# Kernel optimization log

Hardware: AMD Instinct MI355X
Metric: run time of the kernel (lower is better)

The kernel has to match this reference:

```python
import jax, jax.numpy as jnp
import numpy as np
import math

N_TOK = 8192; IN_DIM = 1024; D = 512; HEADS = 8; DH = D // HEADS
M = D // 2; ITERS = 6; SCALE = DH ** -0.5; KRES = 33; NCLS = 2
EPS = 1e-5


def ln(x, g, b):
    mu = jnp.mean(x, -1, keepdims=True)
    var = jnp.var(x, -1, keepdims=True)
    return (x - mu) * jax.lax.rsqrt(var + EPS) * g + b


def moore_penrose_pinv(x):
    # Newton-Schulz iterative pseudo-inverse (lucidrains nystrom-attention)
    col = jnp.abs(x).sum(-1).max()
    row = jnp.abs(x).sum(-2).max()
    z = jnp.swapaxes(x, -1, -2) / (col * row)
    I = jnp.eye(x.shape[-1], dtype=x.dtype)
    for _ in range(ITERS):
        xz = x @ z
        z = 0.25 * z @ (13 * I - xz @ (15 * I - xz @ (7 * I - xz)))
    return z


def nystrom_attn(x, qkv_w, out_w, out_b, conv_w):
    b, n, _ = x.shape
    pad = (-n) % M  # pad at FRONT so seq len divisible by num_landmarks
    xp = jnp.pad(x, ((0, 0), (pad, 0), (0, 0)))
    Np = n + pad
    q, k, v = jnp.split(xp @ qkv_w, 3, axis=-1)
    tohead = lambda t: t.reshape(b, Np, HEADS, DH).transpose(0, 2, 1, 3)  # bhnd
    q = tohead(q) * SCALE; k = tohead(k); v = tohead(v)
    l = Np // M
    q_l = q.reshape(b, HEADS, M, l, DH).mean(3)  # landmark means, bhmd
    k_l = k.reshape(b, HEADS, M, l, DH).mean(3)
    a1 = jax.nn.softmax(jnp.einsum('bhnd,bhmd->bhnm', q, k_l), -1)
    a2 = jax.nn.softmax(jnp.einsum('bhnd,bhmd->bhnm', q_l, k_l), -1)
    a3 = jax.nn.softmax(jnp.einsum('bhmd,bhnd->bhmn', q_l, k), -1)
    out = (a1 @ moore_penrose_pinv(a2)) @ (a3 @ v)
    pc = KRES // 2  # depthwise residual conv over sequence dim (groups=heads)
    out = out + jax.lax.conv_general_dilated(
        v, conv_w, (1, 1), [(pc, pc), (0, 0)],
        dimension_numbers=('NCHW', 'OIHW', 'NCHW'), feature_group_count=HEADS)
    out = out.transpose(0, 2, 1, 3).reshape(b, Np, D)
    return (out @ out_w + out_b)[:, -n:]


def ppeg(x, Hs, Ws, w7, b7, w5, b5, w3, b3):
    b, _, C = x.shape
    cls_tok, feat = x[:, :1], x[:, 1:]
    f = feat.transpose(0, 2, 1).reshape(b, C, Hs, Ws)
    def dw(w, bb, p):
        return jax.lax.conv_general_dilated(
            f, w, (1, 1), [(p, p), (p, p)],
            dimension_numbers=('NCHW', 'OIHW', 'NCHW'),
            feature_group_count=C) + bb[None, :, None, None]
    y = f + dw(w7, b7, 3) + dw(w5, b5, 2) + dw(w3, b3, 1)
    y = y.reshape(b, C, Hs * Ws).transpose(0, 2, 1)
    return jnp.concatenate([cls_tok, y], axis=1)


def setup_inputs() -> dict:
    key = jax.random.key(0)
    ks = jax.random.split(key, 16)
    s = 0.02
    return {
        'x': jax.random.normal(ks[0], (N_TOK, IN_DIM), jnp.float32),
        'fc1_w': jax.random.normal(ks[1], (IN_DIM, D), jnp.float32) * s,
        'fc1_b': jnp.zeros((D,), jnp.float32),
        'cls_token': jax.random.normal(ks[2], (1, 1, D), jnp.float32),
        'ln1_g': jnp.ones((D,), jnp.float32), 'ln1_b': jnp.zeros((D,), jnp.float32),
        'qkv1_w': jax.random.normal(ks[3], (D, 3 * D), jnp.float32) * s,
        'out1_w': jax.random.normal(ks[4], (D, D), jnp.float32) * s,
        'out1_b': jnp.zeros((D,), jnp.float32),
        'conv1_w': jax.random.normal(ks[5], (HEADS, 1, KRES, 1), jnp.float32) * s,
        'ln2_g': jnp.ones((D,), jnp.float32), 'ln2_b': jnp.zeros((D,), jnp.float32),
        'qkv2_w': jax.random.normal(ks[6], (D, 3 * D), jnp.float32) * s,
        'out2_w': jax.random.normal(ks[7], (D, D), jnp.float32) * s,
        'out2_b': jnp.zeros((D,), jnp.float32),
        'conv2_w': jax.random.normal(ks[8], (HEADS, 1, KRES, 1), jnp.float32) * s,
        'pg7_w': jax.random.normal(ks[9], (D, 1, 7, 7), jnp.float32) * s,
        'pg7_b': jnp.zeros((D,), jnp.float32),
        'pg5_w': jax.random.normal(ks[10], (D, 1, 5, 5), jnp.float32) * s,
        'pg5_b': jnp.zeros((D,), jnp.float32),
        'pg3_w': jax.random.normal(ks[11], (D, 1, 3, 3), jnp.float32) * s,
        'pg3_b': jnp.zeros((D,), jnp.float32),
        'norm_g': jnp.ones((D,), jnp.float32), 'norm_b': jnp.zeros((D,), jnp.float32),
        'fc2_w': jax.random.normal(ks[12], (D, NCLS), jnp.float32) * s,
        'fc2_b': jnp.zeros((NCLS,), jnp.float32),
    }


def reference(x, fc1_w, fc1_b, cls_token, ln1_g, ln1_b, qkv1_w, out1_w, out1_b,
              conv1_w, ln2_g, ln2_b, qkv2_w, out2_w, out2_b, conv2_w,
              pg7_w, pg7_b, pg5_w, pg5_b, pg3_w, pg3_b, norm_g, norm_b,
              fc2_w, fc2_b):
    h = jax.nn.relu(x[None].astype(jnp.float32) @ fc1_w + fc1_b)  # [1,N,D]
    n = h.shape[1]
    Hs = Ws = int(math.ceil(math.sqrt(n)))
    add = Hs * Ws - n
    h = jnp.concatenate([h, h[:, :add]], axis=1)  # pad to square by duplication
    h = jnp.concatenate([jnp.broadcast_to(cls_token, (1, 1, D)), h], axis=1)
    h = h + nystrom_attn(ln(h, ln1_g, ln1_b), qkv1_w, out1_w, out1_b, conv1_w)
    h = ppeg(h, Hs, Ws, pg7_w, pg7_b, pg5_w, pg5_b, pg3_w, pg3_b)
    h = h + nystrom_attn(ln(h, ln2_g, ln2_b), qkv2_w, out2_w, out2_b, conv2_w)
    emb = ln(h, norm_g, norm_b)[:, 0]  # cls embedding [1,D]
    logits = emb @ fc2_w + fc2_b
    Y_prob = jax.nn.softmax(logits, -1)
    Y_hat = jnp.argmax(logits, -1)
    return (logits, Y_prob, Y_hat, emb)
```

## Files before the change

kernel.cpp:

```cpp
#include <hip/hip_runtime.h>
#include <math.h>

#define NTOK   8192
#define INDIM  1024
#define NHEAD  8
#define N1     8282
#define NP     8448
#define PAD    166
#define LCH    33
#define SCALE  0.125f
#define HS     91
#define KSPLIT 24
#define KCH    (NP / KSPLIT)

typedef __attribute__((ext_vector_type(8))) _Float16 half8;
typedef __attribute__((ext_vector_type(8))) short short8;
typedef __attribute__((ext_vector_type(4))) float f32x4;
typedef unsigned short ushort_t;

#define GPTR(p) ((const __attribute__((address_space(1))) void*)(p))
#define LPTR(p) ((__attribute__((address_space(3))) void*)(p))

__device__ __forceinline__ ushort_t f2h(float f) {
    union { _Float16 h; ushort_t u; } v; v.h = (_Float16)f;
    return v.u;
}
__device__ __forceinline__ float h2f(ushort_t u) {
    union { ushort_t u; _Float16 h; } v; v.u = u;
    return (float)v.h;
}


__device__ __forceinline__ float blockReduceSumF(float v, float* red, int tid) {
    red[tid] = v; __syncthreads();
    for (int s = 128; s > 0; s >>= 1) {
        if (tid < s) red[tid] += red[tid + s];
        __syncthreads();
    }
    float r = red[0]; __syncthreads();
    return r;
}
__device__ __forceinline__ float blockReduceMaxF(float v, float* red, int tid) {
    red[tid] = v; __syncthreads();
    for (int s = 128; s > 0; s >>= 1) {
        if (tid < s) red[tid] = fmaxf(red[tid], red[tid + s]);
        __syncthreads();
    }
    float r = red[0]; __syncthreads();
    return r;
}

__global__ void zero_k(float* __restrict__ p)
{
    int i = blockIdx.x * 256 + threadIdx.x;
    reinterpret_cast<float4*>(p)[i] = make_float4(0.f, 0.f, 0.f, 0.f);
}

__global__ __launch_bounds__(256) void tcast_k(const float* __restrict__ w, ushort_t* __restrict__ wT,
                                               int K, int N)
{
    __shared__ float tb[32][33];
    int tx = threadIdx.x & 31, ty = threadIdx.x >> 5;
    int n0 = blockIdx.x * 32, k0 = blockIdx.y * 32;
#pragma unroll
    for (int i = 0; i < 4; ++i)
        tb[ty + i * 8][tx] = w[(size_t)(k0 + ty + i * 8) * N + n0 + tx];
    __syncthreads();
#pragma unroll
    for (int i = 0; i < 4; ++i)
        wT[(size_t)(n0 + ty + i * 8) * K + k0 + tx] = f2h(tb[tx][ty + i * 8]);
}

__global__ void bcast_k(const float* __restrict__ x, ushort_t* __restrict__ o)
{
    int i = blockIdx.x * 256 + threadIdx.x;
    float4 v = reinterpret_cast<const float4*>(x)[i];
    ushort4 u;
    u.x = f2h(v.x); u.y = f2h(v.y); u.z = f2h(v.z); u.w = f2h(v.w);
    reinterpret_cast<ushort4*>(o)[i] = u;
}

__global__ __launch_bounds__(256) void gemm_mn_f16(
    const ushort_t* __restrict__ A, const ushort_t* __restrict__ BT,
    const float* __restrict__ bias, const float* __restrict__ res,
    float* __restrict__ C, ushort_t* __restrict__ Ch,
    int Mvalid, int K, int lda, int ldb, int ldc, int relu, int qscale)
{
    __shared__ ushort_t As[128 * 32];
    __shared__ ushort_t Bs[64 * 32];
    const int tid = threadIdx.x;
    const int wave = tid >> 6, lane = tid & 63;
    const int row0 = blockIdx.y * 128, col0 = blockIdx.x * 64;
    const int wr = wave * 32;
    const int aRow = wave * 16 + (lane >> 2);
    const int aChS = (((lane & 3) ^ ((lane >> 3) & 3)) * 8);
    const int bRow = tid >> 2;
    const int bChS = (((tid & 3) ^ ((tid >> 3) & 3)) * 8);
    const int lr = lane & 15, lq = (lane >> 4) * 4;
    const int lks = (((lane >> 4) ^ ((lr >> 1) & 3)) * 8);
    f32x4 acc[2][4] = {};
    for (int k0 = 0; k0 < K; k0 += 32) {
        __syncthreads();
#pragma unroll
        for (int i = 0; i < 2; ++i) {
            const ushort_t* gp = A + (size_t)(row0 + i * 64 + aRow) * lda + k0 + aChS;
            __builtin_amdgcn_global_load_lds(GPTR(gp), LPTR(As + (i * 64 + wave * 16) * 32), 16, 0, 0);
        }
        const ushort_t* gq = BT + (size_t)(col0 + bRow) * ldb + k0 + bChS;
        __builtin_amdgcn_global_load_lds(GPTR(gq), LPTR(Bs + tid * 8), 16, 0, 0);
        __syncthreads();
        half8 af[2], bfr[4];
#pragma unroll
        for (int mi = 0; mi < 2; ++mi)
            af[mi] = *reinterpret_cast<const half8*>(&As[(wr + mi * 16 + lr) * 32 + lks]);
#pragma unroll
        for (int ni = 0; ni < 4; ++ni)
            bfr[ni] = *reinterpret_cast<const half8*>(&Bs[(ni * 16 + lr) * 32 + lks]);
#pragma unroll
        for (int mi = 0; mi < 2; ++mi)
#pragma unroll
            for (int ni = 0; ni < 4; ++ni)
                acc[mi][ni] = __builtin_amdgcn_mfma_f32_16x16x32_f16(af[mi], bfr[ni], acc[mi][ni], 0, 0, 0);
    }
#pragma unroll
    for (int mi = 0; mi < 2; ++mi) {
#pragma unroll
        for (int q = 0; q < 4; ++q) {
            int r = row0 + wr + mi * 16 + lq + q;
            if (r >= Mvalid) continue;
#pragma unroll
            for (int ni = 0; ni < 4; ++ni) {
                int c = col0 + ni * 16 + lr;
                float v = acc[mi][ni][q];
                if (bias) v += bias[c];
                if (res)  v += res[(size_t)r * ldc + c];
                if (relu) v = fmaxf(v, 0.f);
                if (Ch) {
                    if (qscale && c < 512) v *= SCALE;
                    Ch[(size_t)r * ldc + c] = f2h(v);
                } else {
                    C[(size_t)r * ldc + c] = v;
                }
            }
        }
    }
}

__global__ __launch_bounds__(256) void bgemm64_f16(
    const ushort_t* __restrict__ A, const ushort_t* __restrict__ B,
    ushort_t* __restrict__ C, float diag, float ss,
    ushort_t* __restrict__ C2, float diag2, float ss2)
{
    __shared__ ushort_t As[64 * 32];
    __shared__ ushort_t Bs[64 * 32];
    const int h = blockIdx.z;
    const ushort_t* Ah = A + (size_t)h * 65536;
    const ushort_t* Bh = B + (size_t)h * 65536;
    const int tid = threadIdx.x;
    const int wave = tid >> 6, lane = tid & 63;
    const int row0 = blockIdx.y * 64, col0 = blockIdx.x * 64;
    const int wr = (wave >> 1) * 32, wc = (wave & 1) * 32;
    const int aRow = tid >> 2;
    const int aChS = (((tid & 3) ^ ((tid >> 3) & 3)) * 8);
    const int kp = (tid >> 3) & 15, nc = tid & 7;
    const int kk = (kp * 2) ^ ((nc & 3) << 3);
    const int lr = lane & 15, lk = (lane >> 4) * 8, lq = (lane >> 4) * 4;
    const int lks = (((lane >> 4) ^ ((lr >> 1) & 3)) * 8);
    f32x4 acc[2][2] = {};
    for (int k0 = 0; k0 < 256; k0 += 32) {
        __syncthreads();
        const ushort_t* gp = Ah + (size_t)(row0 + aRow) * 256 + k0 + aChS;
        __builtin_amdgcn_global_load_lds(GPTR(gp), LPTR(As + tid * 8), 16, 0, 0);
        if (tid < 128) {
            const ushort_t* bp = Bh + (size_t)(k0 + kp * 2) * 256 + col0 + nc * 8;
            short8 v0 = *reinterpret_cast<const short8*>(bp);
            short8 v1 = *reinterpret_cast<const short8*>(bp + 256);
#pragma unroll
            for (int j = 0; j < 8; ++j) {
                unsigned int pk = ((unsigned int)(ushort_t)v1[j] << 16) | (unsigned int)(ushort_t)v0[j];
                *reinterpret_cast<unsigned int*>(&Bs[(nc * 8 + j) * 32 + kk]) = pk;
            }
        }
        __syncthreads();
        half8 af[2], bfr[2];
#pragma unroll
        for (int mi = 0; mi < 2; ++mi)
            af[mi] = *reinterpret_cast<const half8*>(&As[(wr + mi * 16 + lr) * 32 + lks]);
#pragma unroll
        for (int ni = 0; ni < 2; ++ni) {
            int nn = wc + ni * 16 + lr;
            bfr[ni] = *reinterpret_cast<const half8*>(&Bs[nn * 32 + (lk ^ (((nn >> 3) & 3) << 3))]);
        }
#pragma unroll
        for (int mi = 0; mi < 2; ++mi)
#pragma unroll
            for (int ni = 0; ni < 2; ++ni)
                acc[mi][ni] = __builtin_amdgcn_mfma_f32_16x16x32_f16(af[mi], bfr[ni], acc[mi][ni], 0, 0, 0);
    }
    ushort_t* Chp = C + (size_t)h * 65536;
#pragma unroll
    for (int mi = 0; mi < 2; ++mi)
#pragma unroll
        for (int ni = 0; ni < 2; ++ni)
#pragma unroll
            for (int q = 0; q < 4; ++q) {
                int r = row0 + wr + mi * 16 + lq + q;
                int c = col0 + wc + ni * 16 + lr;
                float v = ss * acc[mi][ni][q];
                if (r == c) v += diag;
                Chp[(size_t)r * 256 + c] = f2h(v);
                if (C2) {
                    float v2 = ss2 * acc[mi][ni][q];
                    if (r == c) v2 += diag2;
                    C2[(size_t)h * 65536 + (size_t)r * 256 + c] = f2h(v2);
                }
            }
}

__global__ __launch_bounds__(256) void hgemm_abT_k(
    const ushort_t* __restrict__ A, long sAh, int lda,
    const ushort_t* __restrict__ BT, long sBh, int ldb,
    ushort_t* __restrict__ C, long sCh, int ldc, int K,
    float* __restrict__ rsum, int sRsum)
{
    __shared__ ushort_t As[128 * 32];
    __shared__ ushort_t Bs[128 * 32];
    const int h = blockIdx.z;
    const ushort_t* Ah = A + (size_t)h * sAh;
    const ushort_t* Bh = BT + (size_t)h * sBh;
    ushort_t* Chp = C + (size_t)h * sCh;
    const int tid = threadIdx.x;
    const int wave = tid >> 6, lane = tid & 63;
    const int row0 = blockIdx.y * 128, col0 = blockIdx.x * 128;
    const int wr = (wave >> 1) * 64, wc = (wave & 1) * 64;
    const int sRow = wave * 16 + (lane >> 2);
    const int sChS = (((lane & 3) ^ ((lane >> 3) & 3)) * 8);
    const int lr = lane & 15, lq = (lane >> 4) * 4;
    const int lks = (((lane >> 4) ^ ((lr >> 1) & 3)) * 8);
    f32x4 acc[4][4] = {};
    for (int k0 = 0; k0 < K; k0 += 32) {
        __syncthreads();
#pragma unroll
        for (int i = 0; i < 2; ++i) {
            const ushort_t* gp = Ah + (size_t)(row0 + i * 64 + sRow) * lda + k0 + sChS;
            __builtin_amdgcn_global_load_lds(GPTR(gp), LPTR(As + (i * 64 + wave * 16) * 32), 16, 0, 0);
            const ushort_t* gq = Bh + (size_t)(col0 + i * 64 + sRow) * ldb + k0 + sChS;
            __builtin_amdgcn_global_load_lds(GPTR(gq), LPTR(Bs + (i * 64 + wave * 16) * 32), 16, 0, 0);
        }
        __syncthreads();
        half8 af[4], bfr[4];
#pragma unroll
        for (int mi = 0; mi < 4; ++mi)
            af[mi] = *reinterpret_cast<const half8*>(&As[(wr + mi * 16 + lr) * 32 + lks]);
#pragma unroll
        for (int ni = 0; ni < 4; ++ni)
            bfr[ni] = *reinterpret_cast<const half8*>(&Bs[(wc + ni * 16 + lr) * 32 + lks]);
#pragma unroll
        for (int mi = 0; mi < 4; ++mi)
#pragma unroll
            for (int ni = 0; ni < 4; ++ni)
                acc[mi][ni] = __builtin_amdgcn_mfma_f32_16x16x32_f16(af[mi], bfr[ni], acc[mi][ni], 0, 0, 0);
    }
#pragma unroll
    for (int mi = 0; mi < 4; ++mi)
#pragma unroll
        for (int q = 0; q < 4; ++q) {
            int r = row0 + wr + mi * 16 + lq + q;
            float s = 0.f;
#pragma unroll
            for (int ni = 0; ni < 4; ++ni) {
                float e = __expf(acc[mi][ni][q]);
                Chp[(size_t)r * ldc + col0 + wc + ni * 16 + lr] = f2h(e);
                s += e;
            }
            for (int off = 8; off; off >>= 1) s += __shfl_xor(s, off, 64);
            if (lr == 0) atomicAdd(&rsum[(size_t)h * sRsum + r], s);
        }
}

__global__ __launch_bounds__(256) void hgemm_pv_k(
    const ushort_t* __restrict__ P, const ushort_t* __restrict__ qkv16,
    float* __restrict__ part)
{
    __shared__ ushort_t As[128 * 32];
    __shared__ ushort_t Bs[64 * 32];
    const int ks = blockIdx.x, row0 = blockIdx.y * 128, h = blockIdx.z;
    const ushort_t* Ph = P + (size_t)h * 256 * NP;
    const ushort_t* V = qkv16 + 1024 + h * 64;
    const int tid = threadIdx.x;
    const int wave = tid >> 6, lane = tid & 63;
    const int wr = wave * 32;
    const int sRow = wave * 16 + (lane >> 2);
    const int sChS = (((lane & 3) ^ ((lane >> 3) & 3)) * 8);
    const int lr = lane & 15, lk = (lane >> 4) * 8, lq = (lane >> 4) * 4;
    const int lks = (((lane >> 4) ^ ((lr >> 1) & 3)) * 8);
    const int kp = (tid >> 3) & 15, nc = tid & 7;
    const int kk = (kp * 2) ^ ((nc & 3) << 3);
    f32x4 acc[2][4] = {};
    for (int k0 = ks * KCH; k0 < (ks + 1) * KCH; k0 += 32) {
        __syncthreads();
#pragma unroll
        for (int i = 0; i < 2; ++i) {
            const ushort_t* gp = Ph + (size_t)(row0 + i * 64 + sRow) * NP + k0 + sChS;
            __builtin_amdgcn_global_load_lds(GPTR(gp), LPTR(As + (i * 64 + wave * 16) * 32), 16, 0, 0);
        }
        if (tid < 128) {
            const ushort_t* bp = V + (size_t)(k0 + kp * 2) * 1536 + nc * 8;
            short8 v0 = *reinterpret_cast<const short8*>(bp);
            short8 v1 = *reinterpret_cast<const short8*>(bp + 1536);
#pragma unroll
            for (int j = 0; j < 8; ++j) {
                unsigned int pk = ((unsigned int)(ushort_t)v1[j] << 16) | (unsigned int)(ushort_t)v0[j];
                *reinterpret_cast<unsigned int*>(&Bs[(nc * 8 + j) * 32 + kk]) = pk;
            }
        }
        __syncthreads();
        half8 af[2], bfr[4];
#pragma unroll
        for (int mi = 0; mi < 2; ++mi)
            af[mi] = *reinterpret_cast<const half8*>(&As[(wr + mi * 16 + lr) * 32 + lks]);
#pragma unroll
        for (int ni = 0; ni < 4; ++ni) {
            int nn = ni * 16 + lr;
            bfr[ni] = *reinterpret_cast<const half8*>(&Bs[nn * 32 + (lk ^ (((nn >> 3) & 3) << 3))]);
        }
#pragma unroll
        for (int mi = 0; mi < 2; ++mi)
#pragma unroll
            for (int ni = 0; ni < 4; ++ni)
                acc[mi][ni] = __builtin_amdgcn_mfma_f32_16x16x32_f16(af[mi], bfr[ni], acc[mi][ni], 0, 0, 0);
    }
    float* pp = part + ((size_t)(ks * 8 + h) * 256) * 64;
#pragma unroll
    for (int mi = 0; mi < 2; ++mi)
#pragma unroll
        for (int q = 0; q < 4; ++q) {
            int r = row0 + wr + mi * 16 + lq + q;
#pragma unroll
            for (int ni = 0; ni < 4; ++ni)
                pp[(size_t)r * 64 + ni * 16 + lr] = acc[mi][ni][q];
        }
}

__global__ __launch_bounds__(256) void pv_reduce_k(const float* __restrict__ part,
                                                   const float* __restrict__ rsum,
                                                   ushort_t* __restrict__ av)
{
    int idx = blockIdx.x * 256 + threadIdx.x;
    int rc = idx >> 6;
    float s = 0.f;
#pragma unroll
    for (int ks = 0; ks < KSPLIT; ++ks)
        s += part[(size_t)ks * 131072 + idx];
    av[idx] = f2h(s / rsum[rc]);
}

__global__ __launch_bounds__(256) void wmat_k(const ushort_t* __restrict__ z,
                                              const ushort_t* __restrict__ av,
                                              ushort_t* __restrict__ W)
{
    int idx = blockIdx.x * 4 + (threadIdx.x >> 6);
    int h = idx >> 8, m = idx & 255, d = threadIdx.x & 63;
    const ushort_t* zp = z + (size_t)h * 65536 + (size_t)m * 256;
    const ushort_t* ap = av + (size_t)h * 16384 + d;
    float acc = 0.f;
    for (int j = 0; j < 256; ++j) acc += h2f(zp[j]) * h2f(ap[(size_t)j * 64]);
    W[((size_t)h * 256 + m) * 64 + d] = f2h(acc);
}

__global__ __launch_bounds__(256) void hgemm_pw_k(
    const ushort_t* __restrict__ P1, const ushort_t* __restrict__ W,
    const float* __restrict__ rsum, ushort_t* __restrict__ attn)
{
    __shared__ ushort_t As[128 * 32];
    __shared__ ushort_t Bs[64 * 32];
    const int row0 = blockIdx.y * 128, h = blockIdx.z;
    const ushort_t* Ph = P1 + (size_t)h * NP * 256;
    const ushort_t* Wh = W + (size_t)h * 16384;
    const int tid = threadIdx.x;
    const int wave = tid >> 6, lane = tid & 63;
    const int wr = wave * 32;
    const int sRow = wave * 16 + (lane >> 2);
    const int sChS = (((lane & 3) ^ ((lane >> 3) & 3)) * 8);
    const int lr = lane & 15, lk = (lane >> 4) * 8, lq = (lane >> 4) * 4;
    const int lks = (((lane >> 4) ^ ((lr >> 1) & 3)) * 8);
    const int kp = (tid >> 3) & 15, nc = tid & 7;
    const int kk = (kp * 2) ^ ((nc & 3) << 3);
    f32x4 acc[2][4] = {};
    for (int k0 = 0; k0 < 256; k0 += 32) {
        __syncthreads();
#pragma unroll
        for (int i = 0; i < 2; ++i) {
            const ushort_t* gp = Ph + (size_t)(row0 + i * 64 + sRow) * 256 + k0 + sChS;
            __builtin_amdgcn_global_load_lds(GPTR(gp), LPTR(As + (i * 64 + wave * 16) * 32), 16, 0, 0);
        }
        if (tid < 128) {
            const ushort_t* bp = Wh + (size_t)(k0 + kp * 2) * 64 + nc * 8;
            short8 v0 = *reinterpret_cast<const short8*>(bp);
            short8 v1 = *reinterpret_cast<const short8*>(bp + 64);
#pragma unroll
            for (int j = 0; j < 8; ++j) {
                unsigned int pk = ((unsigned int)(ushort_t)v1[j] << 16) | (unsigned int)(ushort_t)v0[j];
                *reinterpret_cast<unsigned int*>(&Bs[(nc * 8 + j) * 32 + kk]) = pk;
            }
        }
        __syncthreads();
        half8 af[2], bfr[4];
#pragma unroll
        for (int mi = 0; mi < 2; ++mi)
            af[mi] = *reinterpret_cast<const half8*>(&As[(wr + mi * 16 + lr) * 32 + lks]);
#pragma unroll
        for (int ni = 0; ni < 4; ++ni) {
            int nn = ni * 16 + lr;
            bfr[ni] = *reinterpret_cast<const half8*>(&Bs[nn * 32 + (lk ^ (((nn >> 3) & 3) << 3))]);
        }
#pragma unroll
        for (int mi = 0; mi < 2; ++mi)
#pragma unroll
            for (int ni = 0; ni < 4; ++ni)
                acc[mi][ni] = __builtin_amdgcn_mfma_f32_16x16x32_f16(af[mi], bfr[ni], acc[mi][ni], 0, 0, 0);
    }
#pragma unroll
    for (int mi = 0; mi < 2; ++mi)
#pragma unroll
        for (int q = 0; q < 4; ++q) {
            int t = row0 + wr + mi * 16 + lq + q;
            float inv = 1.f / rsum[(size_t)h * NP + t];
#pragma unroll
            for (int ni = 0; ni < 4; ++ni)
                attn[(size_t)t * 512 + h * 64 + ni * 16 + lr] = f2h(acc[mi][ni][q] * inv);
        }
}

__global__ void fixup_k(const float* __restrict__ cls, float* __restrict__ h)
{
    int i = blockIdx.x * 256 + threadIdx.x;
    if (i < 512) {
        h[i] = cls[i];
    } else {
        int j = i - 512;
        h[(size_t)8193 * 512 + j] = h[512 + j];
    }
}

__global__ __launch_bounds__(256) void ln_pad_k(
    const float* __restrict__ h, const float* __restrict__ g, const float* __restrict__ b,
    ushort_t* __restrict__ out)
{
    int row = blockIdx.x, tid = threadIdx.x;
    __shared__ float red[256];
    ushort_t* o = out + (size_t)row * 512;
    if (row < PAD) { o[tid] = 0; o[tid + 256] = 0; return; }
    const float* x = h + (size_t)(row - PAD) * 512;
    float v0 = x[tid], v1 = x[tid + 256];
    float mu = blockReduceSumF(v0 + v1, red, tid) * (1.f / 512.f);
    float d0 = v0 - mu, d1 = v1 - mu;
    float var = blockReduceSumF(d0 * d0 + d1 * d1, red, tid) * (1.f / 512.f);
    float rstd = rsqrtf(var + 1e-5f);
    o[tid]       = f2h(d0 * rstd * g[tid] + b[tid]);
    o[tid + 256] = f2h(d1 * rstd * g[tid + 256] + b[tid + 256]);
}

__global__ __launch_bounds__(256) void landmark_k(const ushort_t* __restrict__ qkv,
                                                  ushort_t* __restrict__ ql,
                                                  ushort_t* __restrict__ kl)
{
    int idx = blockIdx.x * 4 + (threadIdx.x >> 6);
    int h = idx >> 8, m = idx & 255, d = threadIdx.x & 63;
    const ushort_t* base = qkv + (size_t)(m * LCH) * 1536 + h * 64 + d;
    float sq = 0.f, sk = 0.f;
    for (int i = 0; i < LCH; ++i) {
        sq += h2f(base[(size_t)i * 1536]);
        sk += h2f(base[(size_t)i * 1536 + 512]);
    }
    ql[((size_t)h * 256 + m) * 64 + d] = f2h(sq * (1.f / (float)LCH));
    kl[((size_t)h * 256 + m) * 64 + d] = f2h(sk * (1.f / (float)LCH));
}

__global__ __launch_bounds__(256) void a2_k(
    const ushort_t* __restrict__ ql, const ushort_t* __restrict__ kl, ushort_t* __restrict__ a2)
{
    int h = blockIdx.x >> 8, r = blockIdx.x & 255, tid = threadIdx.x;
    __shared__ float qv[64]; __shared__ float red[256];
    if (tid < 64) qv[tid] = h2f(ql[((size_t)h * 256 + r) * 64 + tid]);
    __syncthreads();
    const ushort_t* kp = kl + ((size_t)h * 256 + tid) * 64;
    float dot = 0.f;
#pragma unroll
    for (int d = 0; d < 64; ++d) dot += qv[d] * h2f(kp[d]);
    float mx = blockReduceMaxF(dot, red, tid);
    float e = expf(dot - mx);
    float s = blockReduceSumF(e, red, tid);
    a2[((size_t)h * 256 + r) * 256 + tid] = f2h(e / s);
}

__global__ __launch_bounds__(256) void colsum_k(const ushort_t* __restrict__ a2, float* __restrict__ cs)
{
    int h = blockIdx.x >> 8, c = blockIdx.x & 255;
    __shared__ float red[256];
    float v = fabsf(h2f(a2[(size_t)h * 65536 + (size_t)threadIdx.x * 256 + c]));
    float s = blockReduceSumF(v, red, threadIdx.x);
    if (!threadIdx.x) cs[blockIdx.x] = s;
}
__global__ __launch_bounds__(256) void pinv_scal_k(const float* __restrict__ cs, float* __restrict__ scal)
{
    int tid = threadIdx.x; __shared__ float red[256];
    float m2 = -1e30f;
    for (int i = tid; i < 2048; i += 256) m2 = fmaxf(m2, cs[i]);
    m2 = blockReduceMaxF(m2, red, tid);
    if (!tid) scal[0] = 1.f / m2;
}
__global__ __launch_bounds__(256) void zinit_k(const ushort_t* __restrict__ a2, const float* __restrict__ scal,
                                               ushort_t* __restrict__ z)
{
    int h = blockIdx.x >> 8, r = blockIdx.x & 255, c = threadIdx.x;
    z[(size_t)h * 65536 + (size_t)r * 256 + c] =
        f2h(h2f(a2[(size_t)h * 65536 + (size_t)c * 256 + r]) * scal[0]);
}

#define CTT 64
__global__ __launch_bounds__(256) void conv2_k(const ushort_t* __restrict__ qkv,
                                               const float* __restrict__ cw,
                                               ushort_t* __restrict__ attn)
{
    __shared__ float vt[CTT + 32][64];
    int t0 = blockIdx.x * CTT;
    int h = blockIdx.y;
    int tid = threadIdx.x;
    for (int s = tid; s < (CTT + 32) * 8; s += 256) {
        int row = s >> 3, q8 = s & 7;
        int tt = t0 - 16 + row;
        if (tt >= 0 && tt < NP) {
            short8 v = *reinterpret_cast<const short8*>(qkv + (size_t)tt * 1536 + 1024 + h * 64 + q8 * 8);
#pragma unroll
            for (int j = 0; j < 8; ++j) vt[row][q8 * 8 + j] = h2f((ushort_t)v[j]);
        } else {
#pragma unroll
            for (int j = 0; j < 8; ++j) vt[row][q8 * 8 + j] = 0.f;
        }
    }
    float w33[33];
#pragma unroll
    for (int j = 0; j < 33; ++j) w33[j] = cw[h * 33 + j];
    __syncthreads();
    int c = tid & 63, tr = tid >> 6;
    float win[48];
#pragma unroll
    for (int j = 0; j < 48; ++j) win[j] = vt[tr * 16 + j][c];
#pragma unroll
    for (int i = 0; i < 16; ++i) {
        float acc = 0.f;
#pragma unroll
        for (int j = 0; j < 33; ++j) acc += w33[j] * win[i + j];
        size_t idx = (size_t)(t0 + tr * 16 + i) * 512 + h * 64 + c;
        attn[idx] = f2h(h2f(attn[idx]) + acc);
    }
}

#define PTS  16
#define PIT  22
#define PITT (PIT*PIT)
#define PCG  8
#define PSTR 12
__global__ __launch_bounds__(256) void ppeg_tiled_k(
    const float* __restrict__ hin,
    const float* __restrict__ w7, const float* __restrict__ b7,
    const float* __restrict__ w5, const float* __restrict__ b5,
    const float* __restrict__ w3, const float* __restrict__ b3,
    float* __restrict__ hout)
{
    __shared__ float inb[PITT][PSTR];
    __shared__ float wcT[49][PCG];
    __shared__ float bs[PCG];
    int tid = threadIdx.x;
    int c0 = blockIdx.z * PCG;
    int ty0 = blockIdx.y * PTS, tx0 = blockIdx.x * PTS;
    if (blockIdx.x == 0 && blockIdx.y == 0 && tid < PCG)
        hout[c0 + tid] = hin[c0 + tid];
    for (int idx = tid; idx < PITT * 2; idx += 256) {
        int tok = idx >> 1, q = idx & 1;
        int gy = ty0 - 3 + tok / PIT, gx = tx0 - 3 + tok % PIT;
        float4 v = make_float4(0.f, 0.f, 0.f, 0.f);
        if (gy >= 0 && gy < HS && gx >= 0 && gx < HS)
            v = *reinterpret_cast<const float4*>(hin + (size_t)(1 + gy * HS + gx) * 512 + c0 + q * 4);
        *reinterpret_cast<float4*>(&inb[tok][q * 4]) = v;
    }
    for (int idx = tid; idx < PCG * 49; idx += 256) {
        int c = idx / 49, t = idx % 49;
        int ky = t / 7, kx = t % 7, dy = ky - 3, dx = kx - 3;
        float w = w7[(size_t)(c0 + c) * 49 + t];
        if (dy >= -2 && dy <= 2 && dx >= -2 && dx <= 2)
            w += w5[(size_t)(c0 + c) * 25 + (dy + 2) * 5 + (dx + 2)];
        if (dy >= -1 && dy <= 1 && dx >= -1 && dx <= 1)
            w += w3[(size_t)(c0 + c) * 9 + (dy + 1) * 3 + (dx + 1)];
        wcT[t][c] = w;
    }
    if (tid < PCG) bs[tid] = b7[c0 + tid] + b5[c0 + tid] + b3[c0 + tid];
    __syncthreads();
    int oy = tid >> 4, ox = tid & 15;
    int gy = ty0 + oy, gx = tx0 + ox;
    if (gy >= HS || gx >= HS) return;
    float acc[PCG];
    {
        const float* cp = &inb[(oy + 3) * PIT + ox + 3][0];
        float4 i0 = *reinterpret_cast<const float4*>(cp);
        float4 i1 = *reinterpret_cast<const float4*>(cp + 4);
        acc[0] = i0.x + bs[0]; acc[1] = i0.y + bs[1]; acc[2] = i0.z + bs[2]; acc[3] = i0.w + bs[3];
        acc[4] = i1.x + bs[4]; acc[5] = i1.y + bs[5]; acc[6] = i1.z + bs[6]; acc[7] = i1.w + bs[7];
    }
#pragma unroll
    for (int ky = 0; ky < 7; ++ky)
#pragma unroll
        for (int kx = 0; kx < 7; ++kx) {
            int t = ky * 7 + kx;
            const float* dp = &inb[(oy + ky) * PIT + ox + kx][0];
            float4 d0 = *reinterpret_cast<const float4*>(dp);
            float4 d1 = *reinterpret_cast<const float4*>(dp + 4);
            float4 w0 = *reinterpret_cast<const float4*>(&wcT[t][0]);
            float4 w1 = *reinterpret_cast<const float4*>(&wcT[t][4]);
            acc[0] += w0.x * d0.x; acc[1] += w0.y * d0.y;
            acc[2] += w0.z * d0.z; acc[3] += w0.w * d0.w;
            acc[4] += w1.x * d1.x; acc[5] += w1.y * d1.y;
            acc[6] += w1.z * d1.z; acc[7] += w1.w * d1.w;
        }
    float* out = hout + (size_t)(1 + gy * HS + gx) * 512 + c0;
    *reinterpret_cast<float4*>(out)     = make_float4(acc[0], acc[1], acc[2], acc[3]);
    *reinterpret_cast<float4*>(out + 4) = make_float4(acc[4], acc[5], acc[6], acc[7]);
}

__global__ __launch_bounds__(256) void final_k(const float* __restrict__ h,
                                               const float* __restrict__ g, const float* __restrict__ bb,
                                               const float* __restrict__ w, const float* __restrict__ fb,
                                               float* __restrict__ out)
{
    __shared__ float red[256];
    int tid = threadIdx.x;
    float v0 = h[tid], v1 = h[tid + 256];
    float mu = blockReduceSumF(v0 + v1, red, tid) * (1.f / 512.f);
    float d0 = v0 - mu, d1 = v1 - mu;
    float var = blockReduceSumF(d0 * d0 + d1 * d1, red, tid) * (1.f / 512.f);
    float rstd = rsqrtf(var + 1e-5f);
    float e0 = d0 * rstd * g[tid] + bb[tid];
    float e1 = d1 * rstd * g[tid + 256] + bb[tid + 256];
    out[5 + tid] = e0;
    out[5 + 256 + tid] = e1;
    float l0p = e0 * w[tid * 2] + e1 * w[(tid + 256) * 2];
    float l1p = e0 * w[tid * 2 + 1] + e1 * w[(tid + 256) * 2 + 1];
    float l0 = blockReduceSumF(l0p, red, tid);
    float l1 = blockReduceSumF(l1p, red, tid);
    if (!tid) {
        l0 += fb[0]; l1 += fb[1];
        out[0] = l0; out[1] = l1;
        float mx = fmaxf(l0, l1);
        float p0 = expf(l0 - mx), p1 = expf(l1 - mx);
        float si = 1.f / (p0 + p1);
        out[2] = p0 * si; out[3] = p1 * si;
        out[4] = (l1 > l0) ? 1.f : 0.f;
    }
}

struct WsPtrs {
    float *h, *h2, *cs, *scal, *rsum3, *rsum1, *part;
    ushort_t *xbB, *qkv16, *ql16, *kl16, *a2h, *zh, *z2h, *xzh, *t1h, *t2h;
    ushort_t *av16, *W16, *qkvT, *outT, *x16, *fc1T, *S16;
};

static void run_attn(float* hbuf, const float* ln_g, const float* ln_b,
                     const float* qkv_w, const float* out_w, const float* out_b,
                     const float* conv_w, const WsPtrs& P, hipStream_t s)
{
    tcast_k<<<dim3(1536 / 32, 512 / 32), 256, 0, s>>>(qkv_w, P.qkvT, 512, 1536);
    tcast_k<<<dim3(512 / 32, 512 / 32), 256, 0, s>>>(out_w, P.outT, 512, 512);
    ln_pad_k<<<NP, 256, 0, s>>>(hbuf, ln_g, ln_b, P.xbB);
    gemm_mn_f16<<<dim3(1536 / 64, NP / 128), 256, 0, s>>>(P.xbB, P.qkvT, nullptr, nullptr,
                                                          nullptr, P.qkv16, NP, 512, 512, 512, 1536, 0, 1);
    landmark_k<<<512, 256, 0, s>>>(P.qkv16, P.ql16, P.kl16);
    a2_k<<<2048, 256, 0, s>>>(P.ql16, P.kl16, P.a2h);
    colsum_k<<<2048, 256, 0, s>>>(P.a2h, P.cs);
    pinv_scal_k<<<1, 256, 0, s>>>(P.cs, P.scal);
    zinit_k<<<2048, 256, 0, s>>>(P.a2h, P.scal, P.zh);
    ushort_t* za = P.zh; ushort_t* zb = P.z2h;
    for (int it = 0; it < 6; ++it) {
        bgemm64_f16<<<dim3(4, 4, 8), 256, 0, s>>>(P.a2h, za, P.xzh, 0.f, 1.f, P.t1h, 7.f, -1.f);
        bgemm64_f16<<<dim3(4, 4, 8), 256, 0, s>>>(P.xzh, P.t1h, P.t2h, 15.f, -1.f, nullptr, 0.f, 0.f);
        bgemm64_f16<<<dim3(4, 4, 8), 256, 0, s>>>(P.xzh, P.t2h, P.t1h, 13.f, -1.f, nullptr, 0.f, 0.f);
        bgemm64_f16<<<dim3(4, 4, 8), 256, 0, s>>>(za, P.t1h, zb, 0.f, 0.25f, nullptr, 0.f, 0.f);
        ushort_t* tmp = za; za = zb; zb = tmp;
    }
    zero_k<<<68, 256, 0, s>>>(P.rsum3);
    hgemm_abT_k<<<dim3(NP / 128, 2, 8), 256, 0, s>>>(P.ql16, 16384, 64,
                                                     P.qkv16 + 512, 64, 1536,
                                                     P.S16, (long)256 * NP, NP, 64,
                                                     P.rsum3, 256);
    hgemm_pv_k<<<dim3(KSPLIT, 2, 8), 256, 0, s>>>(P.S16, P.qkv16, P.part);
    pv_reduce_k<<<512, 256, 0, s>>>(P.part, P.rsum3, P.av16);
    wmat_k<<<512, 256, 0, s>>>(za, P.av16, P.W16);
    hgemm_abT_k<<<dim3(2, NP / 128, 8), 256, 0, s>>>(P.qkv16, 64, 1536,
                                                     P.kl16, 16384, 64,
                                                     P.S16, (long)NP * 256, 256, 64,
                                                     P.rsum1, NP);
    hgemm_pw_k<<<dim3(1, NP / 128, 8), 256, 0, s>>>(P.S16, P.W16, P.rsum1, P.xbB);
    conv2_k<<<dim3(NP / CTT, 8), 256, 0, s>>>(P.qkv16, conv_w, P.xbB);
    gemm_mn_f16<<<dim3(512 / 64, (N1 + 127) / 128), 256, 0, s>>>(P.xbB + (size_t)PAD * 512, P.outT,
                                                                 out_b, hbuf, hbuf, nullptr,
                                                                 N1, 512, 512, 512, 512, 0, 0);
}

extern "C" void kernel_launch(void* const* d_in, const int* in_sizes, int n_in,
                              void* d_out, int out_size, void* d_ws, size_t ws_size,
                              hipStream_t stream)
{
    (void)in_sizes; (void)n_in; (void)out_size; (void)ws_size;
    const float* x       = (const float*)d_in[0];
    const float* fc1_w   = (const float*)d_in[1];
    const float* fc1_b   = (const float*)d_in[2];
    const float* cls_tok = (const float*)d_in[3];
    const float* ln1_g   = (const float*)d_in[4];
    const float* ln1_b   = (const float*)d_in[5];
    const float* qkv1_w  = (const float*)d_in[6];
    const float* out1_w  = (const float*)d_in[7];
    const float* out1_b  = (const float*)d_in[8];
    const float* conv1_w = (const float*)d_in[9];
    const float* ln2_g   = (const float*)d_in[10];
    const float* ln2_b   = (const float*)d_in[11];
    const float* qkv2_w  = (const float*)d_in[12];
    const float* out2_w  = (const float*)d_in[13];
    const float* out2_b  = (const float*)d_in[14];
    const float* conv2_w = (const float*)d_in[15];
    const float* pg7_w   = (const float*)d_in[16];
    const float* pg7_b   = (const float*)d_in[17];
    const float* pg5_w   = (const float*)d_in[18];
    const float* pg5_b   = (const float*)d_in[19];
    const float* pg3_w   = (const float*)d_in[20];
    const float* pg3_b   = (const float*)d_in[21];
    const float* norm_g  = (const float*)d_in[22];
    const float* norm_b  = (const float*)d_in[23];
    const float* fc2_w   = (const float*)d_in[24];
    const float* fc2_b   = (const float*)d_in[25];

    float* ws = (float*)d_ws;
    WsPtrs P;
    float* cur = ws;
    P.h     = cur; cur += (size_t)N1 * 512;
    P.h2    = cur; cur += (size_t)N1 * 512;
    P.xbB   = (ushort_t*)cur; cur += (size_t)NP * 512 / 2;
    P.qkv16 = (ushort_t*)cur; cur += (size_t)NP * 1536 / 2;
    P.ql16  = (ushort_t*)cur; cur += 65536;
    P.kl16  = (ushort_t*)cur; cur += 65536;
    P.a2h   = (ushort_t*)cur; cur += 262144;
    P.zh    = (ushort_t*)cur; cur += 262144;
    P.z2h   = (ushort_t*)cur; cur += 262144;
    P.xzh   = (ushort_t*)cur; cur += 262144;
    P.t1h   = (ushort_t*)cur; cur += 262144;
    P.t2h   = (ushort_t*)cur; cur += 262144;
    P.av16  = (ushort_t*)cur; cur += 65536;
    P.W16   = (ushort_t*)cur; cur += 65536;
    P.cs    = cur; cur += 2048;
    P.scal  = cur; cur += 64;
    P.qkvT  = (ushort_t*)cur; cur += 393216 + 64;
    P.outT  = (ushort_t*)cur; cur += 131072 + 64;
    P.rsum3 = cur; cur += 2048;
    P.rsum1 = cur; cur += (size_t)8 * NP;
    P.part  = cur; cur += (size_t)KSPLIT * 131072;
    P.S16   = (ushort_t*)cur; cur += (size_t)8 * 256 * NP / 2;
    P.x16   = P.S16;
    P.fc1T  = P.S16 + (size_t)NTOK * INDIM;

    bcast_k<<<(NTOK * INDIM) / 1024, 256, 0, stream>>>(x, P.x16);
    tcast_k<<<dim3(512 / 32, 1024 / 32), 256, 0, stream>>>(fc1_w, P.fc1T, 1024, 512);
    gemm_mn_f16<<<dim3(512 / 64, NTOK / 128), 256, 0, stream>>>(P.x16, P.fc1T, fc1_b, nullptr,
                                                                P.h + 512, nullptr,
                                                                NTOK, 1024, 1024, 1024, 512, 1, 0);
    fixup_k<<<180, 256, 0, stream>>>(cls_tok, P.h);
    run_attn(P.h, ln1_g, ln1_b, qkv1_w, out1_w, out1_b, conv1_w, P, stream);
    ppeg_tiled_k<<<dim3(6, 6, 512 / PCG), 256, 0, stream>>>(P.h, pg7_w, pg7_b, pg5_w, pg5_b,
                                                            pg3_w, pg3_b, P.h2);
    run_attn(P.h2, ln2_g, ln2_b, qkv2_w, out2_w, out2_b, conv2_w, P, stream);
    final_k<<<1, 256, 0, stream>>>(P.h2, norm_g, norm_b, fc2_w, fc2_b, (float*)d_out);
}
```

Before: 792.7 us.

## Fuse Q·K_landmark softmax with P·W product into one flash-style kernel

Replaces the two-kernel path that wrote the exp-score matrix (NP x 256 per head) to global memory and then multiplied it by W with a single kernel. Each 128-row block computes its exp scores into LDS, keeps the row sums locally instead of using atomics, and then runs the P·W GEMM directly from LDS. This removes a large fp16 intermediate round trip through HBM, one launch, and the rsum1 buffer and its zeroing. In exchange it uses about 70KB of LDS per block, which limits occupancy, and the grid shrinks to 66x8 blocks.

```diff
diff --git a/kernel.cpp b/kernel.cpp
--- a/kernel.cpp
+++ b/kernel.cpp
@@ -278,6 +278,122 @@
         }
 }
 
+__global__ __launch_bounds__(256) void fa1_k(
+    const ushort_t* __restrict__ qkv16, const ushort_t* __restrict__ kl,
+    const ushort_t* __restrict__ W, ushort_t* __restrict__ attn)
+{
+    __shared__ ushort_t Pl[128][264];
+    __shared__ ushort_t As[128 * 32];
+    __shared__ ushort_t Bs[64 * 32];
+    __shared__ float rs_l[128];
+    const int h = blockIdx.y;
+    const int row0 = blockIdx.x * 128;
+    const ushort_t* Aq = qkv16 + h * 64;
+    const ushort_t* klh = kl + (size_t)h * 16384;
+    const ushort_t* Wh = W + (size_t)h * 16384;
+    const int tid = threadIdx.x;
+    const int wave = tid >> 6, lane = tid & 63;
+    const int wr = wave * 32;
+    const int aRow = wave * 16 + (lane >> 2);
+    const int aChS = (((lane & 3) ^ ((lane >> 3) & 3)) * 8);
+    const int bRow = tid >> 2;
+    const int bChS = (((tid & 3) ^ ((tid >> 3) & 3)) * 8);
+    const int lr = lane & 15, lk = (lane >> 4) * 8, lq = (lane >> 4) * 4;
+    const int lks = (((lane >> 4) ^ ((lr >> 1) & 3)) * 8);
+    const int kp = (tid >> 3) & 15, ncs = tid & 7;
+    const int kk = (kp * 2) ^ ((ncs & 3) << 3);
+    float rs[2][4] = {};
+    for (int nc0 = 0; nc0 < 256; nc0 += 64) {
+        f32x4 acc[2][4] = {};
+        for (int k0 = 0; k0 < 64; k0 += 32) {
+            __syncthreads();
+#pragma unroll
+            for (int i = 0; i < 2; ++i) {
+                const ushort_t* gp = Aq + (size_t)(row0 + i * 64 + aRow) * 1536 + k0 + aChS;
+                __builtin_amdgcn_global_load_lds(GPTR(gp), LPTR(As + (i * 64 + wave * 16) * 32), 16, 0, 0);
+            }
+            const ushort_t* gq = klh + (size_t)(nc0 + bRow) * 64 + k0 + bChS;
+            __builtin_amdgcn_global_load_lds(GPTR(gq), LPTR(Bs + tid * 8), 16, 0, 0);
+            __syncthreads();
+            half8 af[2], bfr[4];
+#pragma unroll
+            for (int mi = 0; mi < 2; ++mi)
+                af[mi] = *reinterpret_cast<const half8*>(&As[(wr + mi * 16 + lr) * 32 + lks]);
+#pragma unroll
+            for (int ni = 0; ni < 4; ++ni)
+                bfr[ni] = *reinterpret_cast<const half8*>(&Bs[(ni * 16 + lr) * 32 + lks]);
+#pragma unroll
+            for (int mi = 0; mi < 2; ++mi)
+#pragma unroll
+                for (int ni = 0; ni < 4; ++ni)
+                    acc[mi][ni] = __builtin_amdgcn_mfma_f32_16x16x32_f16(af[mi], bfr[ni], acc[mi][ni], 0, 0, 0);
+        }
+#pragma unroll
+        for (int mi = 0; mi < 2; ++mi)
+#pragma unroll
+            for (int q = 0; q < 4; ++q) {
+                int r = wr + mi * 16 + lq + q;
+                float s = 0.f;
+#pragma unroll
+                for (int ni = 0; ni < 4; ++ni) {
+                    float e = __expf(acc[mi][ni][q]);
+                    Pl[r][nc0 + ni * 16 + lr] = f2h(e);
+                    s += e;
+                }
+                for (int off = 8; off; off >>= 1) s += __shfl_xor(s, off, 64);
+                rs[mi][q] += s;
+            }
+    }
+    if (lr == 0) {
+#pragma unroll
+        for (int mi = 0; mi < 2; ++mi)
+#pragma unroll
+            for (int q = 0; q < 4; ++q)
+                rs_l[wr + mi * 16 + lq + q] = rs[mi][q];
+    }
+    __syncthreads();
+    f32x4 acc[2][4] = {};
+    for (int k0 = 0; k0 < 256; k0 += 32) {
+        __syncthreads();
+        if (tid < 128) {
+            const ushort_t* bp = Wh + (size_t)(k0 + kp * 2) * 64 + ncs * 8;
+            short8 v0 = *reinterpret_cast<const short8*>(bp);
+            short8 v1 = *reinterpret_cast<const short8*>(bp + 64);
+#pragma unroll
+            for (int j = 0; j < 8; ++j) {
+                unsigned int pk = ((unsigned int)(ushort_t)v1[j] << 16) | (unsigned int)(ushort_t)v0[j];
+                *reinterpret_cast<unsigned int*>(&Bs[(ncs * 8 + j) * 32 + kk]) = pk;
+            }
+        }
+        __syncthreads();
+        half8 af[2], bfr[4];
+#pragma unroll
+        for (int mi = 0; mi < 2; ++mi)
+            af[mi] = *reinterpret_cast<const half8*>(&Pl[wr + mi * 16 + lr][k0 + lk]);
+#pragma unroll
+        for (int ni = 0; ni < 4; ++ni) {
+            int nn = ni * 16 + lr;
+            bfr[ni] = *reinterpret_cast<const half8*>(&Bs[nn * 32 + (lk ^ (((nn >> 3) & 3) << 3))]);
+        }
+#pragma unroll
+        for (int mi = 0; mi < 2; ++mi)
+#pragma unroll
+            for (int ni = 0; ni < 4; ++ni)
+                acc[mi][ni] = __builtin_amdgcn_mfma_f32_16x16x32_f16(af[mi], bfr[ni], acc[mi][ni], 0, 0, 0);
+    }
+#pragma unroll
+    for (int mi = 0; mi < 2; ++mi)
+#pragma unroll
+        for (int q = 0; q < 4; ++q) {
+            int rloc = wr + mi * 16 + lq + q;
+            int t = row0 + rloc;
+            float inv = 1.f / rs_l[rloc];
+#pragma unroll
+            for (int ni = 0; ni < 4; ++ni)
+                attn[(size_t)t * 512 + h * 64 + ni * 16 + lr] = f2h(acc[mi][ni][q] * inv);
+        }
+}
+
 __global__ __launch_bounds__(256) void hgemm_pv_k(
     const ushort_t* __restrict__ P, const ushort_t* __restrict__ qkv16,
     float* __restrict__ part)
@@ -366,70 +482,6 @@
     float acc = 0.f;
     for (int j = 0; j < 256; ++j) acc += h2f(zp[j]) * h2f(ap[(size_t)j * 64]);
     W[((size_t)h * 256 + m) * 64 + d] = f2h(acc);
-}
-
-__global__ __launch_bounds__(256) void hgemm_pw_k(
-    const ushort_t* __restrict__ P1, const ushort_t* __restrict__ W,
-    const float* __restrict__ rsum, ushort_t* __restrict__ attn)
-{
-    __shared__ ushort_t As[128 * 32];
-    __shared__ ushort_t Bs[64 * 32];
-    const int row0 = blockIdx.y * 128, h = blockIdx.z;
-    const ushort_t* Ph = P1 + (size_t)h * NP * 256;
-    const ushort_t* Wh = W + (size_t)h * 16384;
-    const int tid = threadIdx.x;
-    const int wave = tid >> 6, lane = tid & 63;
-    const int wr = wave * 32;
-    const int sRow = wave * 16 + (lane >> 2);
-    const int sChS = (((lane & 3) ^ ((lane >> 3) & 3)) * 8);
-    const int lr = lane & 15, lk = (lane >> 4) * 8, lq = (lane >> 4) * 4;
-    const int lks = (((lane >> 4) ^ ((lr >> 1) & 3)) * 8);
-    const int kp = (tid >> 3) & 15, nc = tid & 7;
-    const int kk = (kp * 2) ^ ((nc & 3) << 3);
-    f32x4 acc[2][4] = {};
-    for (int k0 = 0; k0 < 256; k0 += 32) {
-        __syncthreads();
-#pragma unroll
-        for (int i = 0; i < 2; ++i) {
-            const ushort_t* gp = Ph + (size_t)(row0 + i * 64 + sRow) * 256 + k0 + sChS;
-            __builtin_amdgcn_global_load_lds(GPTR(gp), LPTR(As + (i * 64 + wave * 16) * 32), 16, 0, 0);
-        }
-        if (tid < 128) {
-            const ushort_t* bp = Wh + (size_t)(k0 + kp * 2) * 64 + nc * 8;
-            short8 v0 = *reinterpret_cast<const short8*>(bp);
-            short8 v1 = *reinterpret_cast<const short8*>(bp + 64);
-#pragma unroll
-            for (int j = 0; j < 8; ++j) {
-                unsigned int pk = ((unsigned int)(ushort_t)v1[j] << 16) | (unsigned int)(ushort_t)v0[j];
-                *reinterpret_cast<unsigned int*>(&Bs[(nc * 8 + j) * 32 + kk]) = pk;
-            }
-        }
-        __syncthreads();
-        half8 af[2], bfr[4];
-#pragma unroll
-        for (int mi = 0; mi < 2; ++mi)
-            af[mi] = *reinterpret_cast<const half8*>(&As[(wr + mi * 16 + lr) * 32 + lks]);
-#pragma unroll
-        for (int ni = 0; ni < 4; ++ni) {
-            int nn = ni * 16 + lr;
-            bfr[ni] = *reinterpret_cast<const half8*>(&Bs[nn * 32 + (lk ^ (((nn >> 3) & 3) << 3))]);
-        }
-#pragma unroll
-        for (int mi = 0; mi < 2; ++mi)
-#pragma unroll
-            for (int ni = 0; ni < 4; ++ni)
-                acc[mi][ni] = __builtin_amdgcn_mfma_f32_16x16x32_f16(af[mi], bfr[ni], acc[mi][ni], 0, 0, 0);
-    }
-#pragma unroll
-    for (int mi = 0; mi < 2; ++mi)
-#pragma unroll
-        for (int q = 0; q < 4; ++q) {
-            int t = row0 + wr + mi * 16 + lq + q;
-            float inv = 1.f / rsum[(size_t)h * NP + t];
-#pragma unroll
-            for (int ni = 0; ni < 4; ++ni)
-                attn[(size_t)t * 512 + h * 64 + ni * 16 + lr] = f2h(acc[mi][ni][q] * inv);
-        }
 }
 
 __global__ void fixup_k(const float* __restrict__ cls, float* __restrict__ h)
@@ -660,7 +712,7 @@
 }
 
 struct WsPtrs {
-    float *h, *h2, *cs, *scal, *rsum3, *rsum1, *part;
+    float *h, *h2, *cs, *scal, *rsum3, *part;
     ushort_t *xbB, *qkv16, *ql16, *kl16, *a2h, *zh, *z2h, *xzh, *t1h, *t2h;
     ushort_t *av16, *W16, *qkvT, *outT, *x16, *fc1T, *S16;
 };
@@ -687,7 +739,7 @@
         bgemm64_f16<<<dim3(4, 4, 8), 256, 0, s>>>(za, P.t1h, zb, 0.f, 0.25f, nullptr, 0.f, 0.f);
         ushort_t* tmp = za; za = zb; zb = tmp;
     }
-    zero_k<<<68, 256, 0, s>>>(P.rsum3);
+    zero_k<<<2, 256, 0, s>>>(P.rsum3);
     hgemm_abT_k<<<dim3(NP / 128, 2, 8), 256, 0, s>>>(P.ql16, 16384, 64,
                                                      P.qkv16 + 512, 64, 1536,
                                                      P.S16, (long)256 * NP, NP, 64,
@@ -695,11 +747,7 @@
     hgemm_pv_k<<<dim3(KSPLIT, 2, 8), 256, 0, s>>>(P.S16, P.qkv16, P.part);
     pv_reduce_k<<<512, 256, 0, s>>>(P.part, P.rsum3, P.av16);
     wmat_k<<<512, 256, 0, s>>>(za, P.av16, P.W16);
-    hgemm_abT_k<<<dim3(2, NP / 128, 8), 256, 0, s>>>(P.qkv16, 64, 1536,
-                                                     P.kl16, 16384, 64,
-                                                     P.S16, (long)NP * 256, 256, 64,
-                                                     P.rsum1, NP);
-    hgemm_pw_k<<<dim3(1, NP / 128, 8), 256, 0, s>>>(P.S16, P.W16, P.rsum1, P.xbB);
+    fa1_k<<<dim3(NP / 128, 8), 256, 0, s>>>(P.qkv16, P.kl16, P.W16, P.xbB);
     conv2_k<<<dim3(NP / CTT, 8), 256, 0, s>>>(P.qkv16, conv_w, P.xbB);
     gemm_mn_f16<<<dim3(512 / 64, (N1 + 127) / 128), 256, 0, s>>>(P.xbB + (size_t)PAD * 512, P.outT,
                                                                  out_b, hbuf, hbuf, nullptr,
@@ -760,7 +808,6 @@
     P.qkvT  = (ushort_t*)cur; cur += 393216 + 64;
     P.outT  = (ushort_t*)cur; cur += 131072 + 64;
     P.rsum3 = cur; cur += 2048;
-    P.rsum1 = cur; cur += (size_t)8 * NP;
     P.part  = cur; cur += (size_t)KSPLIT * 131072;
     P.S16   = (ushort_t*)cur; cur += (size_t)8 * 256 * NP / 2;
     P.x16   = P.S16;
```

Measured after the change: 782.4 us. Within noise of the previous version (-1.3%).
